# Performance work log

Hardware: AMD Instinct MI355X
Metric: run time of the kernel (lower is better)

The kernel has to match this reference:

```python
import jax, jax.numpy as jnp
import numpy as np

NUM_HEADS = 12


def setup_inputs() -> dict:
    key = jax.random.key(0)
    k0, k1, k2 = jax.random.split(key, 3)
    B, N, C = 32, 864, 768  # N = 2*t_h*t_w + s_h*s_w = 288 + 576
    x = jax.random.normal(k0, (B, N, C), dtype=jnp.float32)
    W_qkv = jax.random.normal(k1, (C, 3 * C), dtype=jnp.float32) * 0.02
    W_proj = jax.random.normal(k2, (C, C), dtype=jnp.float32) * 0.02
    b_proj = jnp.zeros((C,), dtype=jnp.float32)
    return {"x": x, "W_qkv": W_qkv, "W_proj": W_proj, "b_proj": b_proj,
            "t_h": 12, "t_w": 12, "s_h": 24, "s_w": 24}


def reference(x, W_qkv, W_proj, b_proj, t_h, t_w, s_h, s_w):
    B, N, C = x.shape
    H = NUM_HEADS
    d = C // H
    scale = d ** -0.5
    # qkv projection (no bias), shape [3, B, H, N, d]
    qkv = (x @ W_qkv).reshape(B, N, 3, H, d).transpose(2, 0, 3, 1, 4)
    q, k, v = qkv[0], qkv[1], qkv[2]
    Tt = 2 * t_h * t_w            # temporal (template) query tokens = 288
    Ts = s_h * s_w                # spatial (search) query tokens = 576
    Mt = 2 * ((t_h + 1) // 2) ** 2  # sub-sampled temporal kv tokens = 72
    Ms = (s_h * s_w) // 4           # sub-sampled spatial kv tokens = 144
    q_t, q_s = q[:, :, :Tt], q[:, :, Tt:Tt + Ts]
    k_t, k_s = k[:, :, :Mt], k[:, :, Mt:Mt + Ms]
    v_t, v_s = v[:, :, :Mt], v[:, :, Mt:Mt + Ms]
    # temporal queries attend spatial keys/values
    a_t = jax.nn.softmax(jnp.einsum('bhqd,bhkd->bhqk', q_t, k_s) * scale, axis=-1)
    x_t = jnp.einsum('bhqk,bhkd->bhqd', a_t, v_s).transpose(0, 2, 1, 3).reshape(B, Tt, C)
    # spatial queries attend temporal keys/values
    a_s = jax.nn.softmax(jnp.einsum('bhqd,bhkd->bhqk', q_s, k_t) * scale, axis=-1)
    x_s = jnp.einsum('bhqk,bhkd->bhqd', a_s, v_t).transpose(0, 2, 1, 3).reshape(B, Ts, C)
    out = jnp.concatenate([x_t, x_s], axis=1)  # [B, N, C]
    return out @ W_proj + b_proj
```

## Files before the change

kernel.cpp:

```cpp
#include <hip/hip_runtime.h>
#include <hip/hip_bf16.h>

typedef __attribute__((ext_vector_type(8))) short short8;
typedef __attribute__((ext_vector_type(4))) float floatx4;

#define MFMA16(a, b, c) __builtin_amdgcn_mfma_f32_16x16x32_bf16((a), (b), (c), 0, 0, 0)

static constexpr int Bb = 32, Nn = 864, Cc = 768, Hh = 12;
static constexpr int Mm = Bb * Nn;
static constexpr int KVROWS = 256;

__device__ __forceinline__ void gload_lds16(const __hip_bfloat16* g, __hip_bfloat16* l) {
    __builtin_amdgcn_global_load_lds((const __attribute__((address_space(1))) void*)g,
                                     (__attribute__((address_space(3))) void*)l, 16, 0, 0);
}

static constexpr int CVT_BLKS = (Mm * Cc / 4) / 256;
static constexpr int TQKV_BLKS = (3 * Cc / 32) * (Cc / 32);
static constexpr int TPROJ_BLKS = (Cc / 32) * (Cc / 32);

__global__ __launch_bounds__(256) void prep_kernel(const float* __restrict__ x,
                                                   const float* __restrict__ Wqkv,
                                                   const float* __restrict__ Wproj,
                                                   __hip_bfloat16* __restrict__ xb,
                                                   __hip_bfloat16* __restrict__ WqkvT,
                                                   __hip_bfloat16* __restrict__ WprojT) {
    __shared__ float tile[32][33];
    const int bx = blockIdx.x;
    if (bx < CVT_BLKS) {
        const int i = bx * 256 + threadIdx.x;
        const float4 v = ((const float4*)x)[i];
        __hip_bfloat16 o[4] = {__float2bfloat16(v.x), __float2bfloat16(v.y),
                               __float2bfloat16(v.z), __float2bfloat16(v.w)};
        ((uint2*)xb)[i] = *(const uint2*)o;
        return;
    }
    const float* in;
    __hip_bfloat16* out;
    int R, C, bid;
    if (bx < CVT_BLKS + TQKV_BLKS) {
        bid = bx - CVT_BLKS; in = Wqkv; out = WqkvT; R = Cc; C = 3 * Cc;
    } else {
        bid = bx - CVT_BLKS - TQKV_BLKS; in = Wproj; out = WprojT; R = Cc; C = Cc;
    }
    const int c0 = (bid % (C / 32)) * 32, r0 = (bid / (C / 32)) * 32;
    const int tx = threadIdx.x & 31, ty = threadIdx.x >> 5;
#pragma unroll
    for (int i = 0; i < 32; i += 8)
        tile[ty + i][tx] = in[(size_t)(r0 + ty + i) * C + c0 + tx];
    __syncthreads();
#pragma unroll
    for (int i = 0; i < 32; i += 8)
        out[(size_t)(c0 + ty + i) * R + r0 + tx] = __float2bfloat16(tile[tx][ty + i]);
}

static constexpr int QBLKS = 6 * (Mm / 128);
static constexpr int KVBLKS = 12 * (Bb * KVROWS / 128);
static constexpr int QKV_NWG = QBLKS + KVBLKS;

__global__ __launch_bounds__(256) void gemm_qkv(const __hip_bfloat16* __restrict__ A,
                                                const __hip_bfloat16* __restrict__ WqkvT,
                                                __hip_bfloat16* __restrict__ Qbuf,
                                                __hip_bfloat16* __restrict__ Kbuf,
                                                __hip_bfloat16* __restrict__ VTbuf) {
    __shared__ __align__(16) char SMEM[34816];
    __hip_bfloat16* As = (__hip_bfloat16*)SMEM;
    __hip_bfloat16* Bs = As + 8192;

    const int braw = (int)blockIdx.x;
    const int sid = (braw & 7) * (QKV_NWG / 8) + (braw >> 3);

    int arow0, orow0, btrow, ncol0, bb = 0, keybase = 0;
    __hip_bfloat16* Out;
    int Nout;
    bool vmode = false;
    if (sid < QBLKS) {
        const int nt = sid % 6, mt = sid / 6;
        arow0 = mt * 128; orow0 = arow0;
        btrow = nt * 128; ncol0 = nt * 128;
        Out = Qbuf; Nout = Cc;
    } else {
        const int s = sid - QBLKS;
        const int nt = s % 12, mt = s / 12;
        bb = mt >> 1; keybase = (mt & 1) << 7;
        arow0 = bb * Nn + keybase;
        btrow = Cc + nt * 128;
        if (nt < 6) {
            orow0 = bb * KVROWS + keybase; ncol0 = nt * 128;
            Out = Kbuf; Nout = Cc;
        } else {
            vmode = true; ncol0 = (nt - 6) * 128;
            Out = nullptr; Nout = 0; orow0 = 0;
        }
    }

    const int t = threadIdx.x;
    const int lane = t & 63, wave = t >> 6;
    const int wm = (wave >> 1) * 64, wn = (wave & 1) * 64;
    const int ln = lane & 15, quad = lane >> 4;

    floatx4 acc[4][4] = {};

    const int r0 = t >> 2;
    const int cst = (t & 3) * 8;
    const __hip_bfloat16* Ag = A + (size_t)(arow0 + r0) * Cc + cst;
    const __hip_bfloat16* Bg = WqkvT + (size_t)(btrow + r0) * Cc + cst;
    const size_t rowskip = (size_t)64 * Cc;

    for (int k0 = 0; k0 < Cc; k0 += 64) {
        gload_lds16(Ag + k0,                &As[t * 8]);
        gload_lds16(Ag + k0 + rowskip,      &As[2048 + t * 8]);
        gload_lds16(Ag + k0 + 32,           &As[4096 + t * 8]);
        gload_lds16(Ag + k0 + 32 + rowskip, &As[6144 + t * 8]);
        gload_lds16(Bg + k0,                &Bs[t * 8]);
        gload_lds16(Bg + k0 + rowskip,      &Bs[2048 + t * 8]);
        gload_lds16(Bg + k0 + 32,           &Bs[4096 + t * 8]);
        gload_lds16(Bg + k0 + 32 + rowskip, &Bs[6144 + t * 8]);
        __syncthreads();

#pragma unroll
        for (int s = 0; s < 2; s++) {
            short8 af[4], bfr[4];
#pragma unroll
            for (int i = 0; i < 4; i++)
                af[i] = *(const short8*)&As[s * 4096 + (wm + i * 16 + ln) * 32 + quad * 8];
#pragma unroll
            for (int j = 0; j < 4; j++)
                bfr[j] = *(const short8*)&Bs[s * 4096 + (wn + j * 16 + ln) * 32 + quad * 8];
#pragma unroll
            for (int i = 0; i < 4; i++)
#pragma unroll
                for (int j = 0; j < 4; j++)
                    acc[i][j] = MFMA16(af[i], bfr[j], acc[i][j]);
        }
        __syncthreads();
    }

    if (!vmode) {
#pragma unroll
        for (int j = 0; j < 4; j++) {
            const int n = ncol0 + wn + j * 16 + ln;
#pragma unroll
            for (int i = 0; i < 4; i++) {
                const int mrow = orow0 + wm + i * 16 + quad * 4;
#pragma unroll
                for (int r = 0; r < 4; r++)
                    Out[(size_t)(mrow + r) * Nout + n] = __float2bfloat16(acc[i][j][r]);
            }
        }
        return;
    }

    __hip_bfloat16* T = (__hip_bfloat16*)SMEM;
#pragma unroll
    for (int j = 0; j < 4; j++) {
        const int ddl = wn + j * 16 + ln;
#pragma unroll
        for (int i = 0; i < 4; i++) {
            const int key = wm + i * 16 + quad * 4;
#pragma unroll
            for (int r = 0; r < 4; r++)
                T[ddl * 136 + key + r] = __float2bfloat16(acc[i][j][r]);
        }
    }
    __syncthreads();
#pragma unroll
    for (int it = 0; it < 8; it++) {
        const int ldd = it * 16 + (t >> 4);
        const int kk = (t & 15) * 8;
        const short8 v = *(const short8*)&T[ldd * 136 + kk];
        *(short8*)&VTbuf[(size_t)(bb * Cc + ncol0 + ldd) * KVROWS + keybase + kk] = v;
    }
}

__global__ __launch_bounds__(256) void gemm_proj(const __hip_bfloat16* __restrict__ A,
                                                 const __hip_bfloat16* __restrict__ BT,
                                                 float* __restrict__ Cout,
                                                 const float* __restrict__ bias) {
    __shared__ __align__(16) __hip_bfloat16 As[8192];
    __shared__ __align__(16) __hip_bfloat16 Bs[8192];
    const int gx = (int)gridDim.x;
    const int nwg = gx * (int)gridDim.y;
    const int braw = (int)blockIdx.y * gx + (int)blockIdx.x;
    const int sid = (braw & 7) * (nwg >> 3) + (braw >> 3);
    const int mt = sid / gx, nt = sid - mt * gx;
    const int m0 = mt << 7, n0 = nt * 128;
    const int t = threadIdx.x;
    const int lane = t & 63, wave = t >> 6;
    const int wm = (wave >> 1) * 64, wn = (wave & 1) * 64;
    const int ln = lane & 15, quad = lane >> 4;

    floatx4 acc[4][4] = {};
    const int r0 = t >> 2, cst = (t & 3) * 8;
    const __hip_bfloat16* Ag = A + (size_t)(m0 + r0) * Cc + cst;
    const __hip_bfloat16* Bg = BT + (size_t)(n0 + r0) * Cc + cst;
    const size_t rowskip = (size_t)64 * Cc;

    for (int k0 = 0; k0 < Cc; k0 += 64) {
        gload_lds16(Ag + k0,                &As[t * 8]);
        gload_lds16(Ag + k0 + rowskip,      &As[2048 + t * 8]);
        gload_lds16(Ag + k0 + 32,           &As[4096 + t * 8]);
        gload_lds16(Ag + k0 + 32 + rowskip, &As[6144 + t * 8]);
        gload_lds16(Bg + k0,                &Bs[t * 8]);
        gload_lds16(Bg + k0 + rowskip,      &Bs[2048 + t * 8]);
        gload_lds16(Bg + k0 + 32,           &Bs[4096 + t * 8]);
        gload_lds16(Bg + k0 + 32 + rowskip, &Bs[6144 + t * 8]);
        __syncthreads();
#pragma unroll
        for (int s = 0; s < 2; s++) {
            short8 af[4], bfr[4];
#pragma unroll
            for (int i = 0; i < 4; i++)
                af[i] = *(const short8*)&As[s * 4096 + (wm + i * 16 + ln) * 32 + quad * 8];
#pragma unroll
            for (int j = 0; j < 4; j++)
                bfr[j] = *(const short8*)&Bs[s * 4096 + (wn + j * 16 + ln) * 32 + quad * 8];
#pragma unroll
            for (int i = 0; i < 4; i++)
#pragma unroll
                for (int j = 0; j < 4; j++)
                    acc[i][j] = MFMA16(af[i], bfr[j], acc[i][j]);
        }
        __syncthreads();
    }
#pragma unroll
    for (int j = 0; j < 4; j++) {
        const int n = n0 + wn + j * 16 + ln;
        const float bv = bias[n];
#pragma unroll
        for (int i = 0; i < 4; i++) {
            const int mrow = m0 + wm + i * 16 + quad * 4;
#pragma unroll
            for (int r = 0; r < 4; r++)
                Cout[(size_t)(mrow + r) * Cc + n] = acc[i][j][r] + bv;
        }
    }
}

template <int L, int QOFF, int KVOFF, int NCH>
__device__ __forceinline__ void attn_pair(const __hip_bfloat16* __restrict__ qb,
                                          const __hip_bfloat16* __restrict__ kb,
                                          const __hip_bfloat16* __restrict__ vtb,
                                          __hip_bfloat16* __restrict__ attn,
                                          int p, int h, int b) {
    const int lane = threadIdx.x & 63;
    const int ln = lane & 15, quad = lane >> 4;

    const __hip_bfloat16* kbase = kb + (size_t)(b * KVROWS + KVOFF) * Cc + h * 64;
    const __hip_bfloat16* vtbase = vtb + (size_t)(b * Cc + h * 64) * KVROWS + KVOFF;

    const int qt0 = 2 * p;
    const __hip_bfloat16* qrowA =
        qb + (size_t)(b * Nn + QOFF + qt0 * 16 + ln) * Cc + h * 64;
    const __hip_bfloat16* qrowB = qrowA + (size_t)16 * Cc;
    const short8 aqA0 = *(const short8*)(qrowA + quad * 8);
    const short8 aqA1 = *(const short8*)(qrowA + 32 + quad * 8);
    const short8 aqB0 = *(const short8*)(qrowB + quad * 8);
    const short8 aqB1 = *(const short8*)(qrowB + 32 + quad * 8);

    float dsA = 0.0f, dsB = 0.0f;
    floatx4 accA[4] = {}, accB[4] = {};
    constexpr float CSC = 0.18033688011112042f;

#pragma unroll
    for (int ch = 0; ch < NCH; ch++) {
        unsigned int pkA[2][2] = {}, pkB[2][2] = {};
#pragma unroll
        for (int ti2 = 0; ti2 < 2; ti2++) {
            const int ti = ch * 2 + ti2;
            if (ti * 16 >= L) continue;
            const __hip_bfloat16* krow = kbase + (size_t)(ti * 16 + ln) * Cc;
            const short8 k0 = *(const short8*)(krow + quad * 8);
            const short8 k1 = *(const short8*)(krow + 32 + quad * 8);
            floatx4 sA = {0.f, 0.f, 0.f, 0.f}, sB = {0.f, 0.f, 0.f, 0.f};
            sA = MFMA16(k0, aqA0, sA);
            sA = MFMA16(k1, aqA1, sA);
            sB = MFMA16(k0, aqB0, sB);
            sB = MFMA16(k1, aqB1, sB);
            float pA[4], pB[4];
#pragma unroll
            for (int r = 0; r < 4; r++) {
                float eA = exp2f(sA[r] * CSC);
                float eB = exp2f(sB[r] * CSC);
                if (ti * 16 + 16 > L) {
                    if (ti * 16 + quad * 4 + r >= L) { eA = 0.0f; eB = 0.0f; }
                }
                pA[r] = eA; dsA += eA;
                pB[r] = eB; dsB += eB;
            }
            {
                const __hip_bfloat162 lo = __float22bfloat162_rn(make_float2(pA[0], pA[1]));
                const __hip_bfloat162 hi = __float22bfloat162_rn(make_float2(pA[2], pA[3]));
                pkA[ti2][0] = *(const unsigned int*)&lo;
                pkA[ti2][1] = *(const unsigned int*)&hi;
            }
            {
                const __hip_bfloat162 lo = __float22bfloat162_rn(make_float2(pB[0], pB[1]));
                const __hip_bfloat162 hi = __float22bfloat162_rn(make_float2(pB[2], pB[3]));
                pkB[ti2][0] = *(const unsigned int*)&lo;
                pkB[ti2][1] = *(const unsigned int*)&hi;
            }
        }
        const int srcA = ln + ((quad & 1) << 5);
        const int srcB = srcA + 16;
        const bool hi2 = quad >= 2;
        union { unsigned int u[4]; short8 v; } pfA, pfB;
        {
            const unsigned int c0 = (unsigned int)__shfl((int)pkA[0][0], srcA);
            const unsigned int c1 = (unsigned int)__shfl((int)pkA[0][1], srcA);
            const unsigned int c2 = (unsigned int)__shfl((int)pkA[0][0], srcB);
            const unsigned int c3 = (unsigned int)__shfl((int)pkA[0][1], srcB);
            const unsigned int d0 = (unsigned int)__shfl((int)pkA[1][0], srcA);
            const unsigned int d1 = (unsigned int)__shfl((int)pkA[1][1], srcA);
            const unsigned int d2 = (unsigned int)__shfl((int)pkA[1][0], srcB);
            const unsigned int d3 = (unsigned int)__shfl((int)pkA[1][1], srcB);
            pfA.u[0] = hi2 ? d0 : c0;
            pfA.u[1] = hi2 ? d1 : c1;
            pfA.u[2] = hi2 ? d2 : c2;
            pfA.u[3] = hi2 ? d3 : c3;
        }
        {
            const unsigned int c0 = (unsigned int)__shfl((int)pkB[0][0], srcA);
            const unsigned int c1 = (unsigned int)__shfl((int)pkB[0][1], srcA);
            const unsigned int c2 = (unsigned int)__shfl((int)pkB[0][0], srcB);
            const unsigned int c3 = (unsigned int)__shfl((int)pkB[0][1], srcB);
            const unsigned int d0 = (unsigned int)__shfl((int)pkB[1][0], srcA);
            const unsigned int d1 = (unsigned int)__shfl((int)pkB[1][1], srcA);
            const unsigned int d2 = (unsigned int)__shfl((int)pkB[1][0], srcB);
            const unsigned int d3 = (unsigned int)__shfl((int)pkB[1][1], srcB);
            pfB.u[0] = hi2 ? d0 : c0;
            pfB.u[1] = hi2 ? d1 : c1;
            pfB.u[2] = hi2 ? d2 : c2;
            pfB.u[3] = hi2 ? d3 : c3;
        }
#pragma unroll
        for (int j = 0; j < 4; j++) {
            const short8 vt =
                *(const short8*)&vtbase[(size_t)(j * 16 + ln) * KVROWS + ch * 32 + quad * 8];
            accA[j] = MFMA16(vt, pfA.v, accA[j]);
            accB[j] = MFMA16(vt, pfB.v, accB[j]);
        }
    }

    dsA += __shfl_xor(dsA, 16); dsA += __shfl_xor(dsA, 32);
    dsB += __shfl_xor(dsB, 16); dsB += __shfl_xor(dsB, 32);
    const float invA = 1.0f / dsA, invB = 1.0f / dsB;

    const size_t orowA = (size_t)(b * Nn + QOFF + qt0 * 16 + ln) * Cc + h * 64;
    const size_t orowB = orowA + (size_t)16 * Cc;
#pragma unroll
    for (int j = 0; j < 4; j++) {
        {
            const __hip_bfloat162 lo =
                __float22bfloat162_rn(make_float2(accA[j][0] * invA, accA[j][1] * invA));
            const __hip_bfloat162 hi =
                __float22bfloat162_rn(make_float2(accA[j][2] * invA, accA[j][3] * invA));
            uint2 o = make_uint2(*(const unsigned int*)&lo, *(const unsigned int*)&hi);
            *(uint2*)&attn[orowA + j * 16 + quad * 4] = o;
        }
        {
            const __hip_bfloat162 lo =
                __float22bfloat162_rn(make_float2(accB[j][0] * invB, accB[j][1] * invB));
            const __hip_bfloat162 hi =
                __float22bfloat162_rn(make_float2(accB[j][2] * invB, accB[j][3] * invB));
            uint2 o = make_uint2(*(const unsigned int*)&lo, *(const unsigned int*)&hi);
            *(uint2*)&attn[orowB + j * 16 + quad * 4] = o;
        }
    }
}

static constexpr int ATTN_BLKS = (384 * 27) / 4;

__global__ __launch_bounds__(256) void attn_fused(const __hip_bfloat16* __restrict__ qb,
                                                  const __hip_bfloat16* __restrict__ kb,
                                                  const __hip_bfloat16* __restrict__ vtb,
                                                  __hip_bfloat16* __restrict__ attn) {
    const int rid = (int)blockIdx.x;
    const int vid = (rid & 7) * (ATTN_BLKS / 8) + (rid >> 3);
    const int g = vid * 4 + (threadIdx.x >> 6);
    const int bh = g / 27, slot = g - bh * 27;
    const int h = bh % 12, b = bh / 12;
    if (slot < 9)
        attn_pair<144, 0, 72, 5>(qb, kb, vtb, attn, slot, h, b);
    else
        attn_pair<72, 288, 0, 3>(qb, kb, vtb, attn, slot - 9, h, b);
}

extern "C" void kernel_launch(void* const* d_in, const int* in_sizes, int n_in,
                              void* d_out, int out_size, void* d_ws, size_t ws_size,
                              hipStream_t stream) {
    const float* x     = (const float*)d_in[0];
    const float* Wqkv  = (const float*)d_in[1];
    const float* Wproj = (const float*)d_in[2];
    const float* bproj = (const float*)d_in[3];
    float* out = (float*)d_out;

    char* ws = (char*)d_ws;
    __hip_bfloat16* xb     = (__hip_bfloat16*)ws;
    __hip_bfloat16* WqkvT  = (__hip_bfloat16*)(ws + 42467328);
    __hip_bfloat16* WprojT = (__hip_bfloat16*)(ws + 46006272);
    __hip_bfloat16* Qbuf   = (__hip_bfloat16*)(ws + 47185920);
    __hip_bfloat16* Kbuf   = (__hip_bfloat16*)(ws + 89653248);
    __hip_bfloat16* VTbuf  = (__hip_bfloat16*)(ws + 102236160);
    __hip_bfloat16* attn   = (__hip_bfloat16*)ws;

    prep_kernel<<<CVT_BLKS + TQKV_BLKS + TPROJ_BLKS, 256, 0, stream>>>(x, Wqkv, Wproj, xb,
                                                                       WqkvT, WprojT);
    gemm_qkv<<<QKV_NWG, 256, 0, stream>>>(xb, WqkvT, Qbuf, Kbuf, VTbuf);
    attn_fused<<<ATTN_BLKS, 256, 0, stream>>>(Qbuf, Kbuf, VTbuf, attn);
    gemm_proj<<<dim3(Cc / 128, Mm / 128), 256, 0, stream>>>(attn, WprojT, out, bproj);
}
```

Measured before the change: 343.8 us.

## Store K and V row-major and transpose V in LDS inside attention

The QKV GEMM now writes K and V together as one row-major KV buffer, so the LDS-staged transpose in its epilogue is gone. The attention kernel is reorganised so each block handles one (batch, head, query-chunk). It loads that head's V into LDS with a swizzled, padded transpose, and its waves share it for the PV MFMAs. This removes the global V-transpose pass and the strided VT reads, at the cost of per-block LDS staging, a barrier, and idle waves in partially filled chunks.

Result: faster. 336.8 us (-2.1%).

```diff
diff --git a/kernel.cpp b/kernel.cpp
--- a/kernel.cpp
+++ b/kernel.cpp
@@ -8,6 +8,7 @@
 
 static constexpr int Bb = 32, Nn = 864, Cc = 768, Hh = 12;
 static constexpr int Mm = Bb * Nn;
+static constexpr int NKV = 2 * Cc;
 static constexpr int KVROWS = 256;
 
 __device__ __forceinline__ void gload_lds16(const __hip_bfloat16* g, __hip_bfloat16* l) {
@@ -58,40 +59,32 @@
 static constexpr int KVBLKS = 12 * (Bb * KVROWS / 128);
 static constexpr int QKV_NWG = QBLKS + KVBLKS;
 
-__global__ __launch_bounds__(256) void gemm_qkv(const __hip_bfloat16* __restrict__ A,
-                                                const __hip_bfloat16* __restrict__ WqkvT,
-                                                __hip_bfloat16* __restrict__ Qbuf,
-                                                __hip_bfloat16* __restrict__ Kbuf,
-                                                __hip_bfloat16* __restrict__ VTbuf) {
-    __shared__ __align__(16) char SMEM[34816];
-    __hip_bfloat16* As = (__hip_bfloat16*)SMEM;
-    __hip_bfloat16* Bs = As + 8192;
+__global__ __launch_bounds__(256) void gemm_qkv2(const __hip_bfloat16* __restrict__ A,
+                                                 const __hip_bfloat16* __restrict__ WqkvT,
+                                                 __hip_bfloat16* __restrict__ Qbuf,
+                                                 __hip_bfloat16* __restrict__ KVbuf) {
+    __shared__ __align__(16) __hip_bfloat16 As[8192];
+    __shared__ __align__(16) __hip_bfloat16 Bs[8192];
 
     const int braw = (int)blockIdx.x;
     const int sid = (braw & 7) * (QKV_NWG / 8) + (braw >> 3);
 
-    int arow0, orow0, btrow, ncol0, bb = 0, keybase = 0;
+    int arow0, orow0, btrow0, ncol0, Nout;
     __hip_bfloat16* Out;
-    int Nout;
-    bool vmode = false;
     if (sid < QBLKS) {
         const int nt = sid % 6, mt = sid / 6;
         arow0 = mt * 128; orow0 = arow0;
-        btrow = nt * 128; ncol0 = nt * 128;
+        btrow0 = nt * 128; ncol0 = nt * 128;
         Out = Qbuf; Nout = Cc;
     } else {
         const int s = sid - QBLKS;
         const int nt = s % 12, mt = s / 12;
-        bb = mt >> 1; keybase = (mt & 1) << 7;
+        const int bb = mt >> 1, keybase = (mt & 1) << 7;
         arow0 = bb * Nn + keybase;
-        btrow = Cc + nt * 128;
-        if (nt < 6) {
-            orow0 = bb * KVROWS + keybase; ncol0 = nt * 128;
-            Out = Kbuf; Nout = Cc;
-        } else {
-            vmode = true; ncol0 = (nt - 6) * 128;
-            Out = nullptr; Nout = 0; orow0 = 0;
-        }
+        orow0 = bb * KVROWS + keybase;
+        btrow0 = Cc + nt * 128;
+        ncol0 = nt * 128;
+        Out = KVbuf; Nout = NKV;
     }
 
     const int t = threadIdx.x;
@@ -104,7 +97,7 @@
     const int r0 = t >> 2;
     const int cst = (t & 3) * 8;
     const __hip_bfloat16* Ag = A + (size_t)(arow0 + r0) * Cc + cst;
-    const __hip_bfloat16* Bg = WqkvT + (size_t)(btrow + r0) * Cc + cst;
+    const __hip_bfloat16* Bg = WqkvT + (size_t)(btrow0 + r0) * Cc + cst;
     const size_t rowskip = (size_t)64 * Cc;
 
     for (int k0 = 0; k0 < Cc; k0 += 64) {
@@ -136,40 +129,16 @@
         __syncthreads();
     }
 
-    if (!vmode) {
-#pragma unroll
-        for (int j = 0; j < 4; j++) {
-            const int n = ncol0 + wn + j * 16 + ln;
-#pragma unroll
-            for (int i = 0; i < 4; i++) {
-                const int mrow = orow0 + wm + i * 16 + quad * 4;
-#pragma unroll
-                for (int r = 0; r < 4; r++)
-                    Out[(size_t)(mrow + r) * Nout + n] = __float2bfloat16(acc[i][j][r]);
-            }
-        }
-        return;
-    }
-
-    __hip_bfloat16* T = (__hip_bfloat16*)SMEM;
 #pragma unroll
     for (int j = 0; j < 4; j++) {
-        const int ddl = wn + j * 16 + ln;
+        const int n = ncol0 + wn + j * 16 + ln;
 #pragma unroll
         for (int i = 0; i < 4; i++) {
-            const int key = wm + i * 16 + quad * 4;
+            const int mrow = orow0 + wm + i * 16 + quad * 4;
 #pragma unroll
             for (int r = 0; r < 4; r++)
-                T[ddl * 136 + key + r] = __float2bfloat16(acc[i][j][r]);
-        }
-    }
-    __syncthreads();
-#pragma unroll
-    for (int it = 0; it < 8; it++) {
-        const int ldd = it * 16 + (t >> 4);
-        const int kk = (t & 15) * 8;
-        const short8 v = *(const short8*)&T[ldd * 136 + kk];
-        *(short8*)&VTbuf[(size_t)(bb * Cc + ncol0 + ldd) * KVROWS + keybase + kk] = v;
+                Out[(size_t)(mrow + r) * Nout + n] = __float2bfloat16(acc[i][j][r]);
+        }
     }
 }
 
@@ -237,19 +206,41 @@
     }
 }
 
-template <int L, int QOFF, int KVOFF, int NCH>
+template <int L, int QOFF, int KVOFF, int NQT, int NCH>
 __device__ __forceinline__ void attn_pair(const __hip_bfloat16* __restrict__ qb,
-                                          const __hip_bfloat16* __restrict__ kb,
-                                          const __hip_bfloat16* __restrict__ vtb,
+                                          const __hip_bfloat16* __restrict__ kv,
                                           __hip_bfloat16* __restrict__ attn,
-                                          int p, int h, int b) {
-    const int lane = threadIdx.x & 63;
+                                          int qc, int h, int b,
+                                          __hip_bfloat16* VTs) {
+    constexpr int KPAD = NCH * 32;
+    constexpr int VSTR = KPAD + 8;
+    constexpr int NPAIR = NQT / 2;
+    const int t = threadIdx.x, lane = t & 63, wave = t >> 6;
     const int ln = lane & 15, quad = lane >> 4;
-
-    const __hip_bfloat16* kbase = kb + (size_t)(b * KVROWS + KVOFF) * Cc + h * 64;
-    const __hip_bfloat16* vtbase = vtb + (size_t)(b * Cc + h * 64) * KVROWS + KVOFF;
-
-    const int qt0 = 2 * p;
+    const __hip_bfloat16 z16 = __float2bfloat16(0.0f);
+
+    const __hip_bfloat16* kbase = kv + (size_t)(b * KVROWS + KVOFF) * NKV + h * 64;
+    const __hip_bfloat16* vbase = kbase + Cc;
+
+    for (int c = t; c < KPAD * 8; c += 256) {
+        const int key = c >> 3, s8 = c & 7, d0 = s8 * 8;
+        const int colp = (key + 8 * s8) % KPAD;
+        if (key < L) {
+            uint4 raw = *(const uint4*)(vbase + (size_t)key * NKV + d0);
+            const __hip_bfloat16* pv = (const __hip_bfloat16*)&raw;
+#pragma unroll
+            for (int jj = 0; jj < 8; jj++) VTs[(d0 + jj) * VSTR + colp] = pv[jj];
+        } else {
+#pragma unroll
+            for (int jj = 0; jj < 8; jj++) VTs[(d0 + jj) * VSTR + colp] = z16;
+        }
+    }
+    __syncthreads();
+
+    const int pt = qc * 4 + wave;
+    if (pt >= NPAIR) return;
+
+    const int qt0 = 2 * pt;
     const __hip_bfloat16* qrowA =
         qb + (size_t)(b * Nn + QOFF + qt0 * 16 + ln) * Cc + h * 64;
     const __hip_bfloat16* qrowB = qrowA + (size_t)16 * Cc;
@@ -264,12 +255,16 @@
 
 #pragma unroll
     for (int ch = 0; ch < NCH; ch++) {
-        unsigned int pkA[2][2] = {}, pkB[2][2] = {};
+        unsigned int pkA[2][2], pkB[2][2];
 #pragma unroll
         for (int ti2 = 0; ti2 < 2; ti2++) {
             const int ti = ch * 2 + ti2;
-            if (ti * 16 >= L) continue;
-            const __hip_bfloat16* krow = kbase + (size_t)(ti * 16 + ln) * Cc;
+            if (ti * 16 >= L) {
+                pkA[ti2][0] = 0u; pkA[ti2][1] = 0u;
+                pkB[ti2][0] = 0u; pkB[ti2][1] = 0u;
+                continue;
+            }
+            const __hip_bfloat16* krow = kbase + (size_t)(ti * 16 + ln) * NKV;
             const short8 k0 = *(const short8*)(krow + quad * 8);
             const short8 k1 = *(const short8*)(krow + 32 + quad * 8);
             floatx4 sA = {0.f, 0.f, 0.f, 0.f}, sB = {0.f, 0.f, 0.f, 0.f};
@@ -335,8 +330,9 @@
         }
 #pragma unroll
         for (int j = 0; j < 4; j++) {
-            const short8 vt =
-                *(const short8*)&vtbase[(size_t)(j * 16 + ln) * KVROWS + ch * 32 + quad * 8];
+            const int dd = j * 16 + ln;
+            const int colp = (ch * 32 + quad * 8 + ((dd >> 3) << 3)) % KPAD;
+            const short8 vt = *(const short8*)&VTs[dd * VSTR + colp];
             accA[j] = MFMA16(vt, pfA.v, accA[j]);
             accB[j] = MFMA16(vt, pfB.v, accB[j]);
         }
@@ -369,21 +365,20 @@
     }
 }
 
-static constexpr int ATTN_BLKS = (384 * 27) / 4;
-
-__global__ __launch_bounds__(256) void attn_fused(const __hip_bfloat16* __restrict__ qb,
-                                                  const __hip_bfloat16* __restrict__ kb,
-                                                  const __hip_bfloat16* __restrict__ vtb,
-                                                  __hip_bfloat16* __restrict__ attn) {
-    const int rid = (int)blockIdx.x;
-    const int vid = (rid & 7) * (ATTN_BLKS / 8) + (rid >> 3);
-    const int g = vid * 4 + (threadIdx.x >> 6);
-    const int bh = g / 27, slot = g - bh * 27;
-    const int h = bh % 12, b = bh / 12;
-    if (slot < 9)
-        attn_pair<144, 0, 72, 5>(qb, kb, vtb, attn, slot, h, b);
+static constexpr int ATTN_NB = 8 * Hh * Bb;
+
+__global__ __launch_bounds__(256, 4) void attn_fused(const __hip_bfloat16* __restrict__ qb,
+                                                     const __hip_bfloat16* __restrict__ kv,
+                                                     __hip_bfloat16* __restrict__ attn) {
+    __shared__ __align__(16) __hip_bfloat16 VTs[64 * 168];
+    const int rid = (int)blockIdx.x + 8 * ((int)blockIdx.y + 12 * (int)blockIdx.z);
+    const int vid = (rid & 7) * (ATTN_NB / 8) + (rid >> 3);
+    const int qc = vid % 8, g = vid / 8;
+    const int h = g % 12, bq = g / 12;
+    if (qc < 3)
+        attn_pair<144, 0, 72, 18, 5>(qb, kv, attn, qc, h, bq, VTs);
     else
-        attn_pair<72, 288, 0, 3>(qb, kb, vtb, attn, slot - 9, h, b);
+        attn_pair<72, 288, 0, 36, 3>(qb, kv, attn, qc - 3, h, bq, VTs);
 }
 
 extern "C" void kernel_launch(void* const* d_in, const int* in_sizes, int n_in,
@@ -400,13 +395,12 @@
     __hip_bfloat16* WqkvT  = (__hip_bfloat16*)(ws + 42467328);
     __hip_bfloat16* WprojT = (__hip_bfloat16*)(ws + 46006272);
     __hip_bfloat16* Qbuf   = (__hip_bfloat16*)(ws + 47185920);
-    __hip_bfloat16* Kbuf   = (__hip_bfloat16*)(ws + 89653248);
-    __hip_bfloat16* VTbuf  = (__hip_bfloat16*)(ws + 102236160);
+    __hip_bfloat16* KVbuf  = (__hip_bfloat16*)(ws + 89653248);
     __hip_bfloat16* attn   = (__hip_bfloat16*)ws;
 
     prep_kernel<<<CVT_BLKS + TQKV_BLKS + TPROJ_BLKS, 256, 0, stream>>>(x, Wqkv, Wproj, xb,
                                                                        WqkvT, WprojT);
-    gemm_qkv<<<QKV_NWG, 256, 0, stream>>>(xb, WqkvT, Qbuf, Kbuf, VTbuf);
-    attn_fused<<<ATTN_BLKS, 256, 0, stream>>>(Qbuf, Kbuf, VTbuf, attn);
+    gemm_qkv2<<<QKV_NWG, 256, 0, stream>>>(xb, WqkvT, Qbuf, KVbuf);
+    attn_fused<<<dim3(8, Hh, Bb), 256, 0, stream>>>(Qbuf, KVbuf, attn);
     gemm_proj<<<dim3(Cc / 128, Mm / 128), 256, 0, stream>>>(attn, WprojT, out, bproj);
 }
```
